# Kernel optimization log

Hardware: AMD Instinct MI355X
Metric: run time of the kernel (lower is better)

The kernel has to match this reference:

```python
import jax, jax.numpy as jnp
import numpy as np

EPS = 1e-8
TAU = 0.2  # gumbel temperature


def lorentz_linear(x, W, log_scale):
    # y = W x; project back onto hyperboloid (k=1): time from sigmoid, rescale space
    y = x @ W.T
    time = jax.nn.sigmoid(y[..., :1]) * jnp.exp(log_scale) + 1.1
    narrow = y[..., 1:]
    s = (time * time - 1.0) / jnp.clip(jnp.sum(narrow * narrow, axis=-1, keepdims=True), EPS, None)
    return jnp.concatenate([time, narrow * jnp.sqrt(s)], axis=-1)


def logmap0(x):
    # Lorentz (k=1) log map at origin o=(1,0,...,0): (0, arccosh(x0) * xs/||xs||)
    x0 = x[..., :1]
    xs = x[..., 1:]
    nrm = jnp.clip(jnp.linalg.norm(xs, axis=-1, keepdims=True), EPS, None)
    d = jnp.arccosh(jnp.clip(x0, 1.0 + 1e-6, None))
    return jnp.concatenate([jnp.zeros_like(x0), d * xs / nrm], axis=-1)


def lorentz_dist(a, b):
    # dist = arccosh(-<a,b>_L), <a,b>_L = -a0*b0 + sum_i ai*bi
    inner = a[..., 0] * b[..., 0] - jnp.sum(a[..., 1:] * b[..., 1:], axis=-1)
    return jnp.arccosh(jnp.clip(inner, 1.0 + 1e-6, None))


def scatter_softmax(score, seg, num_segments):
    m = jax.ops.segment_max(score, seg, num_segments=num_segments)
    m = jnp.where(jnp.isfinite(m), m, 0.0)  # empty segments
    e = jnp.exp(score - m[seg])
    s = jax.ops.segment_sum(e, seg, num_segments=num_segments)
    return e / jnp.clip(s[seg], EPS, None)


def setup_inputs() -> dict:
    key = jax.random.key(0)
    ks = jax.random.split(key, 8)
    N, E, D, A = 50000, 800000, 128, 128
    # nodes on hyperboloid: time = sqrt(1 + ||space||^2)
    xs = jax.random.normal(ks[0], (N, D - 1), dtype=jnp.float32)
    x0 = jnp.sqrt(1.0 + jnp.sum(xs * xs, axis=-1, keepdims=True))
    x = jnp.concatenate([x0, xs], axis=-1)
    src = jax.random.randint(ks[1], (E,), 0, N)
    dst = jax.random.randint(ks[2], (E,), 0, N)
    edge_value = jax.random.uniform(ks[3], (E,), dtype=jnp.float32)
    stdv = 1.0 / np.sqrt(D)
    Wq = jax.random.uniform(ks[4], (D, D), minval=-stdv, maxval=stdv, dtype=jnp.float32).at[:, 0].set(0.0)
    Wk = jax.random.uniform(ks[5], (D, D), minval=-stdv, maxval=stdv, dtype=jnp.float32).at[:, 0].set(0.0)
    Wa = jax.random.normal(ks[6], (A, D), dtype=jnp.float32) * np.sqrt(2.0 / (A + D))
    log_scale = jnp.asarray(np.log(10.0), dtype=jnp.float32)
    return {"x": x, "src": src, "dst": dst, "edge_value": edge_value,
            "Wq": Wq, "Wk": Wk, "Wa": Wa,
            "log_scale_q": log_scale, "log_scale_k": log_scale}


def reference(x, src, dst, edge_value, Wq, Wk, Wa, log_scale_q, log_scale_k):
    N = x.shape[0]
    # assignment logits in tangent space -> softmax
    ass = jax.nn.softmax(logmap0(x) @ Wa.T, axis=-1)  # [N, A]
    q = lorentz_linear(x, Wq, log_scale_q)            # [N, D]
    k = lorentz_linear(x, Wk, log_scale_k)
    # per-edge negative Lorentz distance
    score = -lorentz_dist(q[src], k[dst])             # [E]
    # scatter softmax over outgoing edges of each src node
    score = scatter_softmax(score, src, N)
    # sparse attention matmul: out[i] = sum_{e: src=i} score_e * ass[dst_e]
    ass = jax.ops.segment_sum(score[:, None] * ass[dst], src, num_segments=N)  # [N, A]
    # gumbel softmax on log(ass + 1e-6)
    logits = jnp.log(ass + 1e-6)
    u = jax.random.uniform(jax.random.key(42), logits.shape, minval=1e-10, maxval=1.0)
    g = -jnp.log(-jnp.log(u))
    return jax.nn.softmax((logits + g) / TAU, axis=-1)
```

## Files before the change

### kernel.cpp

```cpp
#include <hip/hip_runtime.h>
#include <hip/hip_bf16.h>
#include <hip/hip_fp16.h>
#include <math.h>


#define D128 128
#define XP 136

typedef _Float16 f16x8 __attribute__((ext_vector_type(8)));
typedef float f32x4 __attribute__((ext_vector_type(4)));

__device__ __forceinline__ void threefry2x32(unsigned x0, unsigned x1,
                                             unsigned& o0, unsigned& o1) {
  const unsigned k0 = 0u, k1 = 42u;
  const unsigned k2 = 0x1BD11BDAu ^ k0 ^ k1;
  x0 += k0; x1 += k1;
#define TF_ROT(r) { x0 += x1; x1 = (x1 << (r)) | (x1 >> (32 - (r))); x1 ^= x0; }
  TF_ROT(13) TF_ROT(15) TF_ROT(26) TF_ROT(6)
  x0 += k1; x1 += k2 + 1u;
  TF_ROT(17) TF_ROT(29) TF_ROT(16) TF_ROT(24)
  x0 += k2; x1 += k0 + 2u;
  TF_ROT(13) TF_ROT(15) TF_ROT(26) TF_ROT(6)
  x0 += k0; x1 += k1 + 3u;
  TF_ROT(17) TF_ROT(29) TF_ROT(16) TF_ROT(24)
  x0 += k1; x1 += k2 + 4u;
  TF_ROT(13) TF_ROT(15) TF_ROT(26) TF_ROT(6)
  x0 += k2; x1 += k0 + 5u;
#undef TF_ROT
  o0 = x0; o1 = x1;
}

__device__ __forceinline__ void pack4h(_Float16* dstp, float4 v) {
  union { _Float16 h[4]; uint2 u; } p;
  p.h[0] = (_Float16)v.x; p.h[1] = (_Float16)v.y;
  p.h[2] = (_Float16)v.z; p.h[3] = (_Float16)v.w;
  *reinterpret_cast<uint2*>(dstp) = p.u;
}

__global__ __launch_bounds__(256) void gemm_ass_kernel(
    const float* __restrict__ X, const float* __restrict__ W,
    __half* __restrict__ out, int N) {
  __shared__ __align__(16) char lbuf[64 * XP * 2 + 128 * XP * 2];
  _Float16* xh = (_Float16*)lbuf;
  _Float16* wh = (_Float16*)(lbuf + 64 * XP * 2);
  float* scratch = (float*)(lbuf + 64 * XP * 2);

  const int t = threadIdx.x;
  const int row0 = blockIdx.x * 64;

#pragma unroll
  for (int i = 0; i < 8; ++i) {
    int f = t + 256 * i, r = f >> 5, c4 = f & 31;
    float4 v = make_float4(0.f, 0.f, 0.f, 0.f);
    if (row0 + r < N)
      v = *reinterpret_cast<const float4*>(X + (size_t)(row0 + r) * D128 + c4 * 4);
    *reinterpret_cast<float4*>(&scratch[r * 128 + c4 * 4]) = v;
  }
  __syncthreads();

#pragma unroll
  for (int rr = 0; rr < 2; ++rr) {
    int r = (t >> 3) + 32 * rr, tr = t & 7;
    float ss = 0.f;
    float4 ch[4];
#pragma unroll
    for (int i = 0; i < 4; ++i) {
      ch[i] = *reinterpret_cast<float4*>(&scratch[r * 128 + (tr + 8 * i) * 4]);
      ss += ch[i].x * ch[i].x + ch[i].y * ch[i].y + ch[i].z * ch[i].z + ch[i].w * ch[i].w;
    }
    if (tr == 0) ss -= ch[0].x * ch[0].x;
#pragma unroll
    for (int msk = 1; msk < 8; msk <<= 1) ss += __shfl_xor(ss, msk);
    float x0v = __shfl(ch[0].x, (t & 63) & ~7);
    float dd = acoshf(fmaxf(x0v, 1.f + 1e-6f));
    float sc = dd / fmaxf(sqrtf(ss), 1e-8f);
#pragma unroll
    for (int i = 0; i < 4; ++i) {
      float4 v = ch[i];
      v.x *= sc; v.y *= sc; v.z *= sc; v.w *= sc;
      if (tr == 0 && i == 0) v.x = 0.f;
      *reinterpret_cast<float4*>(&scratch[r * 128 + (tr + 8 * i) * 4]) = v;
    }
  }
  __syncthreads();

#pragma unroll
  for (int i = 0; i < 8; ++i) {
    int f = t + 256 * i, r = f >> 5, c4 = f & 31;
    float4 v = *reinterpret_cast<float4*>(&scratch[r * 128 + c4 * 4]);
    pack4h(&xh[r * XP + c4 * 4], v);
  }
  __syncthreads();

#pragma unroll
  for (int i = 0; i < 16; ++i) {
    int f = t + 256 * i, wr = f >> 5, c4 = f & 31;
    float4 v = *reinterpret_cast<const float4*>(W + (size_t)wr * D128 + c4 * 4);
    pack4h(&wh[wr * XP + c4 * 4], v);
  }
  __syncthreads();

  const int w = t >> 6, lane = t & 63;
  const int lc = lane & 15;
  const int arow = 16 * w + lc;
  const int koff = (lane >> 4) * 8;
  f32x4 acc[8];
#pragma unroll
  for (int i = 0; i < 8; ++i) acc[i] = (f32x4){0.f, 0.f, 0.f, 0.f};

#pragma unroll
  for (int kk = 0; kk < 4; ++kk) {
    f16x8 a = *reinterpret_cast<f16x8*>(&xh[arow * XP + kk * 32 + koff]);
#pragma unroll
    for (int tt = 0; tt < 8; ++tt) {
      f16x8 b = *reinterpret_cast<f16x8*>(&wh[(tt * 16 + lc) * XP + kk * 32 + koff]);
      acc[tt] = __builtin_amdgcn_mfma_f32_16x16x32_f16(a, b, acc[tt], 0, 0, 0);
    }
  }

#pragma unroll
  for (int j = 0; j < 4; ++j) {
    int gr = row0 + 16 * w + ((lane >> 4) << 2) + j;
    float mx = acc[0][j];
#pragma unroll
    for (int tt = 1; tt < 8; ++tt) mx = fmaxf(mx, acc[tt][j]);
#pragma unroll
    for (int msk = 1; msk < 16; msk <<= 1) mx = fmaxf(mx, __shfl_xor(mx, msk));
    float e[8], sm = 0.f;
#pragma unroll
    for (int tt = 0; tt < 8; ++tt) { e[tt] = expf(acc[tt][j] - mx); sm += e[tt]; }
#pragma unroll
    for (int msk = 1; msk < 16; msk <<= 1) sm += __shfl_xor(sm, msk);
    float inv = 1.f / sm;
    if (gr < N) {
#pragma unroll
      for (int tt = 0; tt < 8; ++tt)
        out[(size_t)gr * D128 + tt * 16 + lc] = __float2half(e[tt] * inv);
    }
  }
}

__global__ __launch_bounds__(256) void gemm_qk_kernel(
    const float* __restrict__ X, const float* __restrict__ Wq,
    const float* __restrict__ Wk, const float* __restrict__ lsq,
    const float* __restrict__ lsk, float* __restrict__ qout,
    __half* __restrict__ kout, int N) {
  __shared__ __align__(16) char lbuf[64 * XP * 2 + 128 * XP * 2];
  _Float16* xh = (_Float16*)lbuf;
  _Float16* wh = (_Float16*)(lbuf + 64 * XP * 2);

  const int t = threadIdx.x;
  const int row0 = blockIdx.x * 64;

#pragma unroll
  for (int i = 0; i < 8; ++i) {
    int f = t + 256 * i, r = f >> 5, c4 = f & 31;
    float4 v = make_float4(0.f, 0.f, 0.f, 0.f);
    if (row0 + r < N)
      v = *reinterpret_cast<const float4*>(X + (size_t)(row0 + r) * D128 + c4 * 4);
    pack4h(&xh[r * XP + c4 * 4], v);
  }

  const int w = t >> 6, lane = t & 63;
  const int lc = lane & 15;
  const int arow = 16 * w + lc;
  const int koff = (lane >> 4) * 8;

  for (int pass = 0; pass < 2; ++pass) {
    const float* W = pass ? Wk : Wq;
    if (pass) __syncthreads();
#pragma unroll
    for (int i = 0; i < 16; ++i) {
      int f = t + 256 * i, wr = f >> 5, c4 = f & 31;
      float4 v = *reinterpret_cast<const float4*>(W + (size_t)wr * D128 + c4 * 4);
      pack4h(&wh[wr * XP + c4 * 4], v);
    }
    __syncthreads();

    f32x4 acc[8];
#pragma unroll
    for (int i = 0; i < 8; ++i) acc[i] = (f32x4){0.f, 0.f, 0.f, 0.f};
#pragma unroll
    for (int kk = 0; kk < 4; ++kk) {
      f16x8 a = *reinterpret_cast<f16x8*>(&xh[arow * XP + kk * 32 + koff]);
#pragma unroll
      for (int tt = 0; tt < 8; ++tt) {
        f16x8 b = *reinterpret_cast<f16x8*>(&wh[(tt * 16 + lc) * XP + kk * 32 + koff]);
        acc[tt] = __builtin_amdgcn_mfma_f32_16x16x32_f16(a, b, acc[tt], 0, 0, 0);
      }
    }

    float scale = expf(pass ? lsk[0] : lsq[0]);
#pragma unroll
    for (int j = 0; j < 4; ++j) {
      int gr = row0 + 16 * w + ((lane >> 4) << 2) + j;
      float ss = 0.f;
#pragma unroll
      for (int tt = 0; tt < 8; ++tt) {
        float v = acc[tt][j];
        if (tt == 0 && lc == 0) v = 0.f;
        ss += v * v;
      }
#pragma unroll
      for (int msk = 1; msk < 16; msk <<= 1) ss += __shfl_xor(ss, msk);
      float y0 = __shfl(acc[0][j], lane & ~15);
      float tm = scale / (1.f + expf(-y0)) + 1.1f;
      float qs = sqrtf((tm * tm - 1.f) / fmaxf(ss, 1e-8f));
      if (gr < N) {
        if (pass == 0) {
#pragma unroll
          for (int tt = 0; tt < 8; ++tt) {
            float val = acc[tt][j] * qs;
            if (tt == 0 && lc == 0) val = tm;
            qout[(size_t)gr * D128 + tt * 16 + lc] = val;
          }
        } else {
#pragma unroll
          for (int tt = 0; tt < 8; ++tt) {
            float val = acc[tt][j] * qs;
            if (tt == 0 && lc == 0) val = tm;
            kout[(size_t)gr * D128 + tt * 16 + lc] = __float2half(val);
          }
        }
      }
    }
  }
}

__global__ __launch_bounds__(256) void count_kernel(const int* __restrict__ src,
                                                    int* __restrict__ counts, int E) {
  int e = blockIdx.x * 256 + threadIdx.x;
  if (e < E) atomicAdd(&counts[src[e]], 1);
}

__global__ __launch_bounds__(256) void scan1_kernel(const int* __restrict__ counts,
                                                    int* __restrict__ incl,
                                                    int* __restrict__ partials, int N) {
  int i = blockIdx.x * 256 + threadIdx.x;
  int c = (i < N) ? counts[i] : 0;
  int lane = threadIdx.x & 63, w = threadIdx.x >> 6;
  int v = c;
#pragma unroll
  for (int d = 1; d < 64; d <<= 1) {
    int tv = __shfl_up(v, d);
    if (lane >= d) v += tv;
  }
  __shared__ int wsum[4];
  if (lane == 63) wsum[w] = v;
  __syncthreads();
  int add = 0;
  for (int j = 0; j < w; ++j) add += wsum[j];
  v += add;
  if (i < N) incl[i] = v;
  if (threadIdx.x == 255) partials[blockIdx.x] = v;
}

__global__ __launch_bounds__(256) void scan2_kernel(int* __restrict__ partials, int nparts) {
  int t = threadIdx.x;
  int p = (t < nparts) ? partials[t] : 0;
  int lane = t & 63, w = t >> 6;
  int v = p;
#pragma unroll
  for (int d = 1; d < 64; d <<= 1) {
    int tv = __shfl_up(v, d);
    if (lane >= d) v += tv;
  }
  __shared__ int wsum[4];
  if (lane == 63) wsum[w] = v;
  __syncthreads();
  int add = 0;
  for (int j = 0; j < w; ++j) add += wsum[j];
  v += add;
  if (t < nparts) partials[t] = v - p;
}

__global__ __launch_bounds__(256) void scan3_kernel(const int* __restrict__ counts,
                                                    int* __restrict__ incl_to_start,
                                                    int* __restrict__ cursor,
                                                    const int* __restrict__ partials, int N) {
  int i = blockIdx.x * 256 + threadIdx.x;
  if (i < N) {
    int s = incl_to_start[i] - counts[i] + partials[blockIdx.x];
    incl_to_start[i] = s;
    cursor[i] = s;
  }
}

__global__ __launch_bounds__(256) void csr_fill_kernel(
    const int* __restrict__ src, const int* __restrict__ dst,
    int* __restrict__ cursor, int* __restrict__ dst_s, int E) {
  int e = blockIdx.x * 256 + threadIdx.x;
  if (e < E) {
    int pos = atomicAdd(&cursor[src[e]], 1);
    dst_s[pos] = dst[e];
  }
}

__global__ __launch_bounds__(256) void node_fused_kernel(
    const float* __restrict__ q, const __half* __restrict__ kh,
    const __half* __restrict__ ass, const int* __restrict__ start,
    const int* __restrict__ counts, const int* __restrict__ dst_s,
    float* __restrict__ out, int N) {
  int g = threadIdx.x >> 4;
  int lq = threadIdx.x & 15;
  int n = blockIdx.x * 16 + g;
  if (n >= N) return;
  int st = start[n], deg = counts[n];
  int c8 = lq * 8;

  float4 qa = *reinterpret_cast<const float4*>(q + (size_t)n * D128 + c8);
  float4 qb = *reinterpret_cast<const float4*>(q + (size_t)n * D128 + c8 + 4);

  float lsum = 0.f;
  float acc[8];
#pragma unroll
  for (int j = 0; j < 8; ++j) acc[j] = 0.f;

  if (deg > 0) {
    int d_cur = dst_s[st];
    int d_nxt = (deg > 1) ? dst_s[st + 1] : d_cur;
    uint4 kv = *reinterpret_cast<const uint4*>(kh + (size_t)d_cur * D128 + c8);
    uint4 av = *reinterpret_cast<const uint4*>(ass + (size_t)d_cur * D128 + c8);

    for (int i = 0; i < deg; ++i) {
      uint4 kv_n = *reinterpret_cast<const uint4*>(kh + (size_t)d_nxt * D128 + c8);
      uint4 av_n = *reinterpret_cast<const uint4*>(ass + (size_t)d_nxt * D128 + c8);
      int p2 = st + i + 2;
      int d_nn = dst_s[(p2 < st + deg) ? p2 : st];

      const __half2* kp = reinterpret_cast<const __half2*>(&kv);
      float2 k0 = __half22float2(kp[0]);
      float2 k1 = __half22float2(kp[1]);
      float2 k2 = __half22float2(kp[2]);
      float2 k3 = __half22float2(kp[3]);
      float part = qa.x * k0.x + qa.y * k0.y + qa.z * k1.x + qa.w * k1.y +
                   qb.x * k2.x + qb.y * k2.y + qb.z * k3.x + qb.w * k3.y;
      part = (lq == 0) ? (2.f * qa.x * k0.x - part) : (-part);
#pragma unroll
      for (int msk = 1; msk < 16; msk <<= 1) part += __shfl_xor(part, msk);

      float x = fmaxf(part, 1.f + 1e-6f);
      float tt = x + sqrtf(__builtin_fmaf(x, x, -1.f));
      float w = __builtin_amdgcn_rcpf(tt);

      lsum += w;
      const __half2* hp = reinterpret_cast<const __half2*>(&av);
      float2 v0 = __half22float2(hp[0]);
      float2 v1 = __half22float2(hp[1]);
      float2 v2 = __half22float2(hp[2]);
      float2 v3 = __half22float2(hp[3]);
      acc[0] += w * v0.x;  acc[1] += w * v0.y;
      acc[2] += w * v1.x;  acc[3] += w * v1.y;
      acc[4] += w * v2.x;  acc[5] += w * v2.y;
      acc[6] += w * v3.x;  acc[7] += w * v3.y;

      kv = kv_n; av = av_n;
      d_nxt = d_nn;
    }
  }

  float inv = (deg > 0) ? 1.f / fmaxf(lsum, 1e-8f) : 0.f;

  float vg[8];
#pragma unroll
  for (int j = 0; j < 8; ++j) {
    unsigned o0, o1;
    threefry2x32(0u, (unsigned)(n * D128 + c8 + j), o0, o1);
    unsigned bits = o0 ^ o1;
    float f = __uint_as_float((bits >> 9) | 0x3f800000u) - 1.0f;
    float u = fmaxf(1e-10f, f * (1.0f - 1e-10f) + 1e-10f);
    float gmb = -logf(-logf(u));
    vg[j] = (logf(acc[j] * inv + 1e-6f) + gmb) / 0.2f;
  }
  float mm = vg[0];
#pragma unroll
  for (int j = 1; j < 8; ++j) mm = fmaxf(mm, vg[j]);
#pragma unroll
  for (int msk = 1; msk < 16; msk <<= 1) mm = fmaxf(mm, __shfl_xor(mm, msk));
  float sm = 0.f;
#pragma unroll
  for (int j = 0; j < 8; ++j) { vg[j] = expf(vg[j] - mm); sm += vg[j]; }
#pragma unroll
  for (int msk = 1; msk < 16; msk <<= 1) sm += __shfl_xor(sm, msk);
  float invs = 1.f / sm;
  *reinterpret_cast<float4*>(out + (size_t)n * D128 + c8) =
      make_float4(vg[0] * invs, vg[1] * invs, vg[2] * invs, vg[3] * invs);
  *reinterpret_cast<float4*>(out + (size_t)n * D128 + c8 + 4) =
      make_float4(vg[4] * invs, vg[5] * invs, vg[6] * invs, vg[7] * invs);
}

extern "C" void kernel_launch(void* const* d_in, const int* in_sizes, int n_in,
                              void* d_out, int out_size, void* d_ws, size_t ws_size,
                              hipStream_t stream) {
  const float* x   = (const float*)d_in[0];
  const int*   src = (const int*)d_in[1];
  const int*   dst = (const int*)d_in[2];
  const float* Wq  = (const float*)d_in[4];
  const float* Wk  = (const float*)d_in[5];
  const float* Wa  = (const float*)d_in[6];
  const float* lsq = (const float*)d_in[7];
  const float* lsk = (const float*)d_in[8];
  const int N = in_sizes[0] / D128;
  const int E = in_sizes[1];
  float* out = (float*)d_out;

  float*  qbuf    = (float*)d_ws;
  __half* kbuf    = (__half*)(qbuf + (size_t)N * D128);
  __half* abuf    = kbuf + (size_t)N * D128;
  int*    counts  = (int*)(abuf + (size_t)N * D128);
  int*    startv  = counts + N;
  int*    cursor  = startv + N;
  int*    partials= cursor + N;
  int*    dst_s   = partials + 256;

  hipMemsetAsync(counts, 0, (size_t)N * sizeof(int), stream);

  const int gemm_blocks = (N + 63) / 64;
  gemm_ass_kernel<<<gemm_blocks, 256, 0, stream>>>(x, Wa, abuf, N);
  gemm_qk_kernel<<<gemm_blocks, 256, 0, stream>>>(x, Wq, Wk, lsq, lsk, qbuf, kbuf, N);

  const int eb = (E + 255) / 256;
  count_kernel<<<eb, 256, 0, stream>>>(src, counts, E);

  const int nb = (N + 255) / 256;
  scan1_kernel<<<nb, 256, 0, stream>>>(counts, startv, partials, N);
  scan2_kernel<<<1, 256, 0, stream>>>(partials, nb);
  scan3_kernel<<<nb, 256, 0, stream>>>(counts, startv, cursor, partials, N);
  csr_fill_kernel<<<eb, 256, 0, stream>>>(src, dst, cursor, dst_s, E);

  node_fused_kernel<<<(N + 15) / 16, 256, 0, stream>>>(qbuf, kbuf, abuf, startv,
                                                       counts, dst_s, out, N);
}
```

Before: 225.1 us.

## Pre-convert inputs and weights to fp16, store q in fp16, use fdot2

Adds a conversion kernel that casts x and the three weight matrices to fp16 once, so both GEMM kernels load fp16 directly instead of converting per block. The q projection is now stored as fp16 with the Lorentz sign folded in, letting the edge loop compute the inner product with packed fdot2 instructions. This reduces per-block conversion work and q storage and load bandwidth. It costs an extra launch and an extra pass over x, and lowers precision for x and q.

```diff
diff --git a/kernel.cpp b/kernel.cpp
--- a/kernel.cpp
+++ b/kernel.cpp
@@ -7,8 +7,11 @@
 #define D128 128
 #define XP 136
 
+typedef _Float16 f16x2 __attribute__((ext_vector_type(2)));
 typedef _Float16 f16x8 __attribute__((ext_vector_type(8)));
 typedef float f32x4 __attribute__((ext_vector_type(4)));
+
+union U4 { uint4 u; f16x2 f2[4]; __half2 hh[4]; };
 
 __device__ __forceinline__ void threefry2x32(unsigned x0, unsigned x1,
                                              unsigned& o0, unsigned& o1) {
@@ -30,73 +33,86 @@
   o0 = x0; o1 = x1;
 }
 
-__device__ __forceinline__ void pack4h(_Float16* dstp, float4 v) {
-  union { _Float16 h[4]; uint2 u; } p;
-  p.h[0] = (_Float16)v.x; p.h[1] = (_Float16)v.y;
-  p.h[2] = (_Float16)v.z; p.h[3] = (_Float16)v.w;
-  *reinterpret_cast<uint2*>(dstp) = p.u;
+__global__ __launch_bounds__(256) void cvt_kernel(
+    const float* __restrict__ x, const float* __restrict__ Wq,
+    const float* __restrict__ Wk, const float* __restrict__ Wa,
+    __half* __restrict__ xh, __half* __restrict__ wqh,
+    __half* __restrict__ wkh, __half* __restrict__ wah, int nx8) {
+  int i = blockIdx.x * 256 + threadIdx.x;
+  const float* src; __half* dst; size_t off;
+  if (i < nx8) {
+    src = x; dst = xh; off = (size_t)i * 8;
+  } else {
+    int j = i - nx8; int w = j >> 11; int r = j & 2047;
+    if (w >= 3) return;
+    off = (size_t)r * 8;
+    src = (w == 0) ? Wq : (w == 1) ? Wk : Wa;
+    dst = (w == 0) ? wqh : (w == 1) ? wkh : wah;
+  }
+  float4 a = *reinterpret_cast<const float4*>(src + off);
+  float4 b = *reinterpret_cast<const float4*>(src + off + 4);
+  union { __half2 h2[4]; uint4 u; } pk;
+  pk.h2[0] = __floats2half2_rn(a.x, a.y);
+  pk.h2[1] = __floats2half2_rn(a.z, a.w);
+  pk.h2[2] = __floats2half2_rn(b.x, b.y);
+  pk.h2[3] = __floats2half2_rn(b.z, b.w);
+  *reinterpret_cast<uint4*>(dst + off) = pk.u;
 }
 
 __global__ __launch_bounds__(256) void gemm_ass_kernel(
-    const float* __restrict__ X, const float* __restrict__ W,
+    const __half* __restrict__ xh_g, const __half* __restrict__ wh_g,
     __half* __restrict__ out, int N) {
-  __shared__ __align__(16) char lbuf[64 * XP * 2 + 128 * XP * 2];
-  _Float16* xh = (_Float16*)lbuf;
-  _Float16* wh = (_Float16*)(lbuf + 64 * XP * 2);
-  float* scratch = (float*)(lbuf + 64 * XP * 2);
+  __shared__ __align__(16) _Float16 xs[64 * XP];
+  __shared__ __align__(16) _Float16 wh[128 * XP];
 
   const int t = threadIdx.x;
   const int row0 = blockIdx.x * 64;
 
 #pragma unroll
-  for (int i = 0; i < 8; ++i) {
-    int f = t + 256 * i, r = f >> 5, c4 = f & 31;
-    float4 v = make_float4(0.f, 0.f, 0.f, 0.f);
-    if (row0 + r < N)
-      v = *reinterpret_cast<const float4*>(X + (size_t)(row0 + r) * D128 + c4 * 4);
-    *reinterpret_cast<float4*>(&scratch[r * 128 + c4 * 4]) = v;
-  }
-  __syncthreads();
-
-#pragma unroll
   for (int rr = 0; rr < 2; ++rr) {
     int r = (t >> 3) + 32 * rr, tr = t & 7;
+    int gr = row0 + r;
+    U4 c0, c1;
+    c0.u = make_uint4(0, 0, 0, 0); c1.u = make_uint4(0, 0, 0, 0);
+    if (gr < N) {
+      c0.u = *reinterpret_cast<const uint4*>(xh_g + (size_t)gr * D128 + tr * 16);
+      c1.u = *reinterpret_cast<const uint4*>(xh_g + (size_t)gr * D128 + tr * 16 + 8);
+    }
+    float v[16];
     float ss = 0.f;
-    float4 ch[4];
-#pragma unroll
-    for (int i = 0; i < 4; ++i) {
-      ch[i] = *reinterpret_cast<float4*>(&scratch[r * 128 + (tr + 8 * i) * 4]);
-      ss += ch[i].x * ch[i].x + ch[i].y * ch[i].y + ch[i].z * ch[i].z + ch[i].w * ch[i].w;
-    }
-    if (tr == 0) ss -= ch[0].x * ch[0].x;
+#pragma unroll
+    for (int j = 0; j < 4; ++j) {
+      float2 f = __half22float2(c0.hh[j]);
+      v[2 * j] = f.x; v[2 * j + 1] = f.y; ss += f.x * f.x + f.y * f.y;
+    }
+#pragma unroll
+    for (int j = 0; j < 4; ++j) {
+      float2 f = __half22float2(c1.hh[j]);
+      v[8 + 2 * j] = f.x; v[9 + 2 * j] = f.y; ss += f.x * f.x + f.y * f.y;
+    }
+    if (tr == 0) ss -= v[0] * v[0];
 #pragma unroll
     for (int msk = 1; msk < 8; msk <<= 1) ss += __shfl_xor(ss, msk);
-    float x0v = __shfl(ch[0].x, (t & 63) & ~7);
+    float x0v = __shfl(v[0], (t & 63) & ~7);
     float dd = acoshf(fmaxf(x0v, 1.f + 1e-6f));
     float sc = dd / fmaxf(sqrtf(ss), 1e-8f);
 #pragma unroll
-    for (int i = 0; i < 4; ++i) {
-      float4 v = ch[i];
-      v.x *= sc; v.y *= sc; v.z *= sc; v.w *= sc;
-      if (tr == 0 && i == 0) v.x = 0.f;
-      *reinterpret_cast<float4*>(&scratch[r * 128 + (tr + 8 * i) * 4]) = v;
-    }
-  }
-  __syncthreads();
+    for (int j = 0; j < 16; ++j) v[j] *= sc;
+    if (tr == 0) v[0] = 0.f;
+    union { __half2 h2[4]; uint4 u; } pk;
+#pragma unroll
+    for (int j = 0; j < 4; ++j) pk.h2[j] = __floats2half2_rn(v[2 * j], v[2 * j + 1]);
+    *reinterpret_cast<uint4*>(&xs[r * XP + tr * 16]) = pk.u;
+#pragma unroll
+    for (int j = 0; j < 4; ++j) pk.h2[j] = __floats2half2_rn(v[8 + 2 * j], v[9 + 2 * j]);
+    *reinterpret_cast<uint4*>(&xs[r * XP + tr * 16 + 8]) = pk.u;
+  }
 
 #pragma unroll
   for (int i = 0; i < 8; ++i) {
-    int f = t + 256 * i, r = f >> 5, c4 = f & 31;
-    float4 v = *reinterpret_cast<float4*>(&scratch[r * 128 + c4 * 4]);
-    pack4h(&xh[r * XP + c4 * 4], v);
-  }
-  __syncthreads();
-
-#pragma unroll
-  for (int i = 0; i < 16; ++i) {
-    int f = t + 256 * i, wr = f >> 5, c4 = f & 31;
-    float4 v = *reinterpret_cast<const float4*>(W + (size_t)wr * D128 + c4 * 4);
-    pack4h(&wh[wr * XP + c4 * 4], v);
+    int f = t + 256 * i, wr = f >> 4, c8 = f & 15;
+    *reinterpret_cast<uint4*>(&wh[wr * XP + c8 * 8]) =
+        *reinterpret_cast<const uint4*>(wh_g + (size_t)wr * D128 + c8 * 8);
   }
   __syncthreads();
 
@@ -110,7 +126,7 @@
 
 #pragma unroll
   for (int kk = 0; kk < 4; ++kk) {
-    f16x8 a = *reinterpret_cast<f16x8*>(&xh[arow * XP + kk * 32 + koff]);
+    f16x8 a = *reinterpret_cast<f16x8*>(&xs[arow * XP + kk * 32 + koff]);
 #pragma unroll
     for (int tt = 0; tt < 8; ++tt) {
       f16x8 b = *reinterpret_cast<f16x8*>(&wh[(tt * 16 + lc) * XP + kk * 32 + koff]);
@@ -141,24 +157,23 @@
 }
 
 __global__ __launch_bounds__(256) void gemm_qk_kernel(
-    const float* __restrict__ X, const float* __restrict__ Wq,
-    const float* __restrict__ Wk, const float* __restrict__ lsq,
-    const float* __restrict__ lsk, float* __restrict__ qout,
+    const __half* __restrict__ xh_g, const __half* __restrict__ wqh_g,
+    const __half* __restrict__ wkh_g, const float* __restrict__ lsq,
+    const float* __restrict__ lsk, __half* __restrict__ qout,
     __half* __restrict__ kout, int N) {
-  __shared__ __align__(16) char lbuf[64 * XP * 2 + 128 * XP * 2];
-  _Float16* xh = (_Float16*)lbuf;
-  _Float16* wh = (_Float16*)(lbuf + 64 * XP * 2);
+  __shared__ __align__(16) _Float16 xs[64 * XP];
+  __shared__ __align__(16) _Float16 wh[128 * XP];
 
   const int t = threadIdx.x;
   const int row0 = blockIdx.x * 64;
 
 #pragma unroll
-  for (int i = 0; i < 8; ++i) {
-    int f = t + 256 * i, r = f >> 5, c4 = f & 31;
-    float4 v = make_float4(0.f, 0.f, 0.f, 0.f);
+  for (int i = 0; i < 4; ++i) {
+    int f = t + 256 * i, r = f >> 4, c8 = f & 15;
+    uint4 v = make_uint4(0, 0, 0, 0);
     if (row0 + r < N)
-      v = *reinterpret_cast<const float4*>(X + (size_t)(row0 + r) * D128 + c4 * 4);
-    pack4h(&xh[r * XP + c4 * 4], v);
+      v = *reinterpret_cast<const uint4*>(xh_g + (size_t)(row0 + r) * D128 + c8 * 8);
+    *reinterpret_cast<uint4*>(&xs[r * XP + c8 * 8]) = v;
   }
 
   const int w = t >> 6, lane = t & 63;
@@ -166,14 +181,14 @@
   const int arow = 16 * w + lc;
   const int koff = (lane >> 4) * 8;
 
-  for (int pass = 0; pass < 2; ++pass) {
-    const float* W = pass ? Wk : Wq;
-    if (pass) __syncthreads();
-#pragma unroll
-    for (int i = 0; i < 16; ++i) {
-      int f = t + 256 * i, wr = f >> 5, c4 = f & 31;
-      float4 v = *reinterpret_cast<const float4*>(W + (size_t)wr * D128 + c4 * 4);
-      pack4h(&wh[wr * XP + c4 * 4], v);
+  for (int p = 0; p < 2; ++p) {
+    const __half* Wg = p ? wkh_g : wqh_g;
+    if (p) __syncthreads();
+#pragma unroll
+    for (int i = 0; i < 8; ++i) {
+      int f = t + 256 * i, wr = f >> 4, c8 = f & 15;
+      *reinterpret_cast<uint4*>(&wh[wr * XP + c8 * 8]) =
+          *reinterpret_cast<const uint4*>(Wg + (size_t)wr * D128 + c8 * 8);
     }
     __syncthreads();
 
@@ -182,7 +197,7 @@
     for (int i = 0; i < 8; ++i) acc[i] = (f32x4){0.f, 0.f, 0.f, 0.f};
 #pragma unroll
     for (int kk = 0; kk < 4; ++kk) {
-      f16x8 a = *reinterpret_cast<f16x8*>(&xh[arow * XP + kk * 32 + koff]);
+      f16x8 a = *reinterpret_cast<f16x8*>(&xs[arow * XP + kk * 32 + koff]);
 #pragma unroll
       for (int tt = 0; tt < 8; ++tt) {
         f16x8 b = *reinterpret_cast<f16x8*>(&wh[(tt * 16 + lc) * XP + kk * 32 + koff]);
@@ -190,7 +205,9 @@
       }
     }
 
-    float scale = expf(pass ? lsk[0] : lsq[0]);
+    float scale = expf(p ? lsk[0] : lsq[0]);
+    __half* outp = p ? kout : qout;
+    float sgn = p ? 1.f : -1.f;
 #pragma unroll
     for (int j = 0; j < 4; ++j) {
       int gr = row0 + 16 * w + ((lane >> 4) << 2) + j;
@@ -205,22 +222,13 @@
       for (int msk = 1; msk < 16; msk <<= 1) ss += __shfl_xor(ss, msk);
       float y0 = __shfl(acc[0][j], lane & ~15);
       float tm = scale / (1.f + expf(-y0)) + 1.1f;
-      float qs = sqrtf((tm * tm - 1.f) / fmaxf(ss, 1e-8f));
+      float qs = sqrtf((tm * tm - 1.f) / fmaxf(ss, 1e-8f)) * sgn;
       if (gr < N) {
-        if (pass == 0) {
-#pragma unroll
-          for (int tt = 0; tt < 8; ++tt) {
-            float val = acc[tt][j] * qs;
-            if (tt == 0 && lc == 0) val = tm;
-            qout[(size_t)gr * D128 + tt * 16 + lc] = val;
-          }
-        } else {
-#pragma unroll
-          for (int tt = 0; tt < 8; ++tt) {
-            float val = acc[tt][j] * qs;
-            if (tt == 0 && lc == 0) val = tm;
-            kout[(size_t)gr * D128 + tt * 16 + lc] = __float2half(val);
-          }
+#pragma unroll
+        for (int tt = 0; tt < 8; ++tt) {
+          float val = acc[tt][j] * qs;
+          if (tt == 0 && lc == 0) val = tm;
+          outp[(size_t)gr * D128 + tt * 16 + lc] = __float2half(val);
         }
       }
     }
@@ -297,7 +305,7 @@
 }
 
 __global__ __launch_bounds__(256) void node_fused_kernel(
-    const float* __restrict__ q, const __half* __restrict__ kh,
+    const __half* __restrict__ qh, const __half* __restrict__ kh,
     const __half* __restrict__ ass, const int* __restrict__ start,
     const int* __restrict__ counts, const int* __restrict__ dst_s,
     float* __restrict__ out, int N) {
@@ -308,8 +316,8 @@
   int st = start[n], deg = counts[n];
   int c8 = lq * 8;
 
-  float4 qa = *reinterpret_cast<const float4*>(q + (size_t)n * D128 + c8);
-  float4 qb = *reinterpret_cast<const float4*>(q + (size_t)n * D128 + c8 + 4);
+  U4 qv;
+  qv.u = *reinterpret_cast<const uint4*>(qh + (size_t)n * D128 + c8);
 
   float lsum = 0.f;
   float acc[8];
@@ -319,23 +327,22 @@
   if (deg > 0) {
     int d_cur = dst_s[st];
     int d_nxt = (deg > 1) ? dst_s[st + 1] : d_cur;
-    uint4 kv = *reinterpret_cast<const uint4*>(kh + (size_t)d_cur * D128 + c8);
-    uint4 av = *reinterpret_cast<const uint4*>(ass + (size_t)d_cur * D128 + c8);
+    U4 kv, av;
+    kv.u = *reinterpret_cast<const uint4*>(kh + (size_t)d_cur * D128 + c8);
+    av.u = *reinterpret_cast<const uint4*>(ass + (size_t)d_cur * D128 + c8);
 
     for (int i = 0; i < deg; ++i) {
-      uint4 kv_n = *reinterpret_cast<const uint4*>(kh + (size_t)d_nxt * D128 + c8);
-      uint4 av_n = *reinterpret_cast<const uint4*>(ass + (size_t)d_nxt * D128 + c8);
+      U4 kvn, avn;
+      kvn.u = *reinterpret_cast<const uint4*>(kh + (size_t)d_nxt * D128 + c8);
+      avn.u = *reinterpret_cast<const uint4*>(ass + (size_t)d_nxt * D128 + c8);
       int p2 = st + i + 2;
       int d_nn = dst_s[(p2 < st + deg) ? p2 : st];
 
-      const __half2* kp = reinterpret_cast<const __half2*>(&kv);
-      float2 k0 = __half22float2(kp[0]);
-      float2 k1 = __half22float2(kp[1]);
-      float2 k2 = __half22float2(kp[2]);
-      float2 k3 = __half22float2(kp[3]);
-      float part = qa.x * k0.x + qa.y * k0.y + qa.z * k1.x + qa.w * k1.y +
-                   qb.x * k2.x + qb.y * k2.y + qb.z * k3.x + qb.w * k3.y;
-      part = (lq == 0) ? (2.f * qa.x * k0.x - part) : (-part);
+      float part = __builtin_amdgcn_fdot2(qv.f2[0], kv.f2[0],
+                   __builtin_amdgcn_fdot2(qv.f2[1], kv.f2[1],
+                   __builtin_amdgcn_fdot2(qv.f2[2], kv.f2[2],
+                   __builtin_amdgcn_fdot2(qv.f2[3], kv.f2[3], 0.f, false),
+                   false), false), false);
 #pragma unroll
       for (int msk = 1; msk < 16; msk <<= 1) part += __shfl_xor(part, msk);
 
@@ -344,17 +351,16 @@
       float w = __builtin_amdgcn_rcpf(tt);
 
       lsum += w;
-      const __half2* hp = reinterpret_cast<const __half2*>(&av);
-      float2 v0 = __half22float2(hp[0]);
-      float2 v1 = __half22float2(hp[1]);
-      float2 v2 = __half22float2(hp[2]);
-      float2 v3 = __half22float2(hp[3]);
+      float2 v0 = __half22float2(av.hh[0]);
+      float2 v1 = __half22float2(av.hh[1]);
+      float2 v2 = __half22float2(av.hh[2]);
+      float2 v3 = __half22float2(av.hh[3]);
       acc[0] += w * v0.x;  acc[1] += w * v0.y;
       acc[2] += w * v1.x;  acc[3] += w * v1.y;
       acc[4] += w * v2.x;  acc[5] += w * v2.y;
       acc[6] += w * v3.x;  acc[7] += w * v3.y;
 
-      kv = kv_n; av = av_n;
+      kv = kvn; av = avn;
       d_nxt = d_nn;
     }
   }
@@ -404,20 +410,28 @@
   const int E = in_sizes[1];
   float* out = (float*)d_out;
 
-  float*  qbuf    = (float*)d_ws;
-  __half* kbuf    = (__half*)(qbuf + (size_t)N * D128);
-  __half* abuf    = kbuf + (size_t)N * D128;
-  int*    counts  = (int*)(abuf + (size_t)N * D128);
-  int*    startv  = counts + N;
-  int*    cursor  = startv + N;
-  int*    partials= cursor + N;
-  int*    dst_s   = partials + 256;
+  __half* xh   = (__half*)d_ws;
+  __half* qh   = xh + (size_t)N * D128;
+  __half* kh   = qh + (size_t)N * D128;
+  __half* ah   = kh + (size_t)N * D128;
+  __half* wqh  = ah + (size_t)N * D128;
+  __half* wkh  = wqh + 16384;
+  __half* wah  = wkh + 16384;
+  int* counts  = (int*)(wah + 16384);
+  int* startv  = counts + N;
+  int* cursor  = startv + N;
+  int* partials= cursor + N;
+  int* dst_s   = partials + 256;
 
   hipMemsetAsync(counts, 0, (size_t)N * sizeof(int), stream);
 
+  const int nx8 = N * 16;
+  const int cvt_blocks = (nx8 + 3 * 2048 + 255) / 256;
+  cvt_kernel<<<cvt_blocks, 256, 0, stream>>>(x, Wq, Wk, Wa, xh, wqh, wkh, wah, nx8);
+
   const int gemm_blocks = (N + 63) / 64;
-  gemm_ass_kernel<<<gemm_blocks, 256, 0, stream>>>(x, Wa, abuf, N);
-  gemm_qk_kernel<<<gemm_blocks, 256, 0, stream>>>(x, Wq, Wk, lsq, lsk, qbuf, kbuf, N);
+  gemm_ass_kernel<<<gemm_blocks, 256, 0, stream>>>(xh, wah, ah, N);
+  gemm_qk_kernel<<<gemm_blocks, 256, 0, stream>>>(xh, wqh, wkh, lsq, lsk, qh, kh, N);
 
   const int eb = (E + 255) / 256;
   count_kernel<<<eb, 256, 0, stream>>>(src, counts, E);
@@ -428,6 +442,6 @@
   scan3_kernel<<<nb, 256, 0, stream>>>(counts, startv, cursor, partials, N);
   csr_fill_kernel<<<eb, 256, 0, stream>>>(src, dst, cursor, dst_s, E);
 
-  node_fused_kernel<<<(N + 15) / 16, 256, 0, stream>>>(qbuf, kbuf, abuf, startv,
+  node_fused_kernel<<<(N + 15) / 16, 256, 0, stream>>>(qh, kh, ah, startv,
                                                        counts, dst_s, out, N);
 }
```

After: 213.0 us. 1.06x faster.
